# Kernel tuning notes

Measured on AMD Instinct MI355X. Metric: run time of the kernel, lower is better.

Reference implementation:

```python
import jax, jax.numpy as jnp
import numpy as np

N = 16384
H = 256
C = 2


def setup_inputs() -> dict:
    key = jax.random.key(0)
    ks = jax.random.split(key, 9)
    s = lambda fan_in: 1.0 / np.sqrt(fan_in)
    return {
        "coordinates": jax.random.normal(ks[0], (N, C), dtype=jnp.float32) * 10.0,
        "W1": jax.random.normal(ks[1], (C, H), dtype=jnp.float32) * s(C),
        "b1": jnp.zeros((H,), dtype=jnp.float32),
        "W2": jax.random.normal(ks[2], (H, H), dtype=jnp.float32) * s(H),
        "b2": jnp.zeros((H,), dtype=jnp.float32),
        "Wd1": jax.random.normal(ks[3], (1, H // 2), dtype=jnp.float32) * s(1),
        "bd1": jnp.zeros((H // 2,), dtype=jnp.float32),
        "Wd2": jax.random.normal(ks[4], (H // 2, H), dtype=jnp.float32) * s(H // 2),
        "bd2": jnp.zeros((H,), dtype=jnp.float32),
        "k": 6,
    }


def reference(coordinates, W1, b1, W2, b2, Wd1, bd1, Wd2, bd2, k):
    x = coordinates.astype(jnp.float32)
    # coord MLP: Linear -> SiLU -> Linear
    coord_emb = jax.nn.silu(x @ W1 + b1) @ W2 + b2  # (N, H)

    # pairwise Euclidean distances (N, N), via ||a||^2 + ||b||^2 - 2ab
    sq = jnp.sum(x * x, axis=1)  # (N,)
    d2 = sq[:, None] + sq[None, :] - 2.0 * (x @ x.T)
    dist = jnp.sqrt(jnp.maximum(d2, 1e-12))  # safe sqrt; diag ~ 0

    # k+1 smallest distances per row (includes self at ~0), ascending
    kk = min(k + 1, dist.shape[1])
    neg_top, _ = jax.lax.top_k(-dist, kk)
    topk_dist = -neg_top  # ascending smallest
    mean_dist = jnp.mean(topk_dist[:, 1:], axis=1, keepdims=True)  # (N, 1)

    dist_emb = jax.nn.silu(mean_dist @ Wd1 + bd1) @ Wd2 + bd2  # (N, H)
    return coord_emb + dist_emb
```

## Files before the change

kernel.cpp:

```cpp
#include <hip/hip_runtime.h>
#include <float.h>
#include <math.h>

#define NPTS 16384
#define HDIM 256

#define KNB   256
#define KXMIN (-48.0f)
#define KW    0.375f
#define KINVW (1.0f / KW)
#define NHB   64

typedef __attribute__((ext_vector_type(8))) short bf16x8;
typedef __attribute__((ext_vector_type(4))) float f32x4;

__device__ __forceinline__ float silu_f(float z) {
    return z / (1.0f + __expf(-z));
}

__device__ __forceinline__ short f2bf(float f) {
    unsigned u = __float_as_uint(f);
    u = (u + 0x7FFFu + ((u >> 16) & 1u)) >> 16;
    return (short)u;
}

__device__ __forceinline__ float bcast_lane(float x, int l) {
    return __int_as_float(__builtin_amdgcn_readlane(__float_as_int(x), l));
}

__device__ __forceinline__ int binof(float x) {
    int b = (int)floorf((x - KXMIN) * KINVW);
    return b < 0 ? 0 : (b > KNB - 1 ? KNB - 1 : b);
}

#define INS7(a0,a1,a2,a3,a4,a5,a6,V)                \
    {   const float v_ = (V);                       \
        a6 = fmaxf(a5, fminf(a6, v_));              \
        a5 = fmaxf(a4, fminf(a5, v_));              \
        a4 = fmaxf(a3, fminf(a4, v_));              \
        a3 = fmaxf(a2, fminf(a3, v_));              \
        a2 = fmaxf(a1, fminf(a2, v_));              \
        a1 = fmaxf(a0, fminf(a1, v_));              \
        a0 = fminf(a0, v_);                         \
    }

__global__ __launch_bounds__(256) void prepA_kernel(
        const float* __restrict__ xyf,
        const float* __restrict__ W2, const float* __restrict__ Wd2,
        unsigned short* __restrict__ W2p, unsigned short* __restrict__ Wd2p,
        unsigned* __restrict__ histp) {
    const int tid = threadIdx.x;

    if (blockIdx.x < 48) {
        const int slot = blockIdx.x * 256 + tid;
        const float* src;
        unsigned short* dst;
        int s;
        if (slot < 8192) { src = W2;  dst = W2p;  s = slot; }
        else             { src = Wd2; dst = Wd2p; s = slot - 8192; }
        const int t   = s >> 10;
        const int rem = s & 1023;
        const int ct  = rem >> 6;
        const int l   = rem & 63;
        const int k0  = t * 32 + 8 * (l >> 4);
        const int c   = ct * 16 + (l & 15);
        bf16x8 v;
        #pragma unroll
        for (int i = 0; i < 8; ++i)
            v[i] = f2bf(src[(size_t)(k0 + i) * HDIM + c]);
        ((bf16x8*)dst)[s] = v;
        return;
    }

    __shared__ unsigned lh[KNB];
    const int h = blockIdx.x - 48;
    lh[tid] = 0u;
    __syncthreads();
    atomicAdd(&lh[binof(xyf[2 * (h * 256 + tid)])], 1u);
    __syncthreads();
    histp[h * KNB + tid] = lh[tid];
}

__global__ __launch_bounds__(256) void prepB_kernel(
        const float* __restrict__ xyf,
        const unsigned* __restrict__ histp,
        unsigned* __restrict__ off,
        float2* __restrict__ sxy, unsigned* __restrict__ qidx) {
    __shared__ unsigned sc[KNB];
    __shared__ unsigned cur[KNB];
    const int tid = threadIdx.x;
    const int myb = blockIdx.x;

    unsigned tot = 0u, pre = 0u;
    #pragma unroll
    for (int b = 0; b < NHB; ++b) {
        const unsigned v = histp[b * KNB + tid];
        if (b < myb) pre += v;
        tot += v;
    }
    sc[tid] = tot;
    __syncthreads();
    for (int s = 1; s < KNB; s <<= 1) {
        const unsigned v = (tid >= s) ? sc[tid - s] : 0u;
        __syncthreads();
        sc[tid] += v;
        __syncthreads();
    }
    const unsigned excl = sc[tid] - tot;
    cur[tid] = excl + pre;
    if (myb == 0) {
        off[tid] = excl;
        if (tid == 0) off[KNB] = (unsigned)NPTS;
    }
    __syncthreads();
    const int i = myb * 256 + tid;
    const float2 p = ((const float2*)xyf)[i];
    const unsigned pos = atomicAdd(&cur[binof(p.x)], 1u);
    sxy[pos]  = p;
    qidx[pos] = (unsigned)i;
}

__global__ __launch_bounds__(512, 8) void knn_search(const float2* __restrict__ sxy,
                                                     const unsigned* __restrict__ qidx,
                                                     const unsigned* __restrict__ off,
                                                     float* __restrict__ md) {
    const int lane = threadIdx.x & 63;
    const int wv   = threadIdx.x >> 6;
    const int qpos = blockIdx.x * 8 + wv;
    const float2 q = sxy[qpos];

    float s0 = FLT_MAX, s1 = FLT_MAX, s2 = FLT_MAX, s3 = FLT_MAX,
          s4 = FLT_MAX, s5 = FLT_MAX, s6 = FLT_MAX;

    const int plo = qpos > 256 ? qpos - 256 : 0;
    const int phi = qpos < NPTS - 256 ? qpos + 255 : NPTS - 1;
    const int lb  = binof(sxy[plo].x);
    const int rb  = binof(sxy[phi].x);

    {
        const unsigned o = off[lb], e = off[rb + 1];
        for (unsigned u = o + (unsigned)lane; u < e; u += 64u) {
            const float2 p = sxy[u];
            const float dx = q.x - p.x, dy = q.y - p.y;
            const float d2 = fmaf(dx, dx, dy * dy);
            if (d2 < s6) INS7(s0, s1, s2, s3, s4, s5, s6, d2)
        }
    }

    #pragma unroll
    for (int m = 1; m < 64; m <<= 1) {
        const float o0 = __shfl_xor(s0, m);
        const float o1 = __shfl_xor(s1, m);
        const float o2 = __shfl_xor(s2, m);
        const float o3 = __shfl_xor(s3, m);
        const float o4 = __shfl_xor(s4, m);
        const float o5 = __shfl_xor(s5, m);
        const float o6 = __shfl_xor(s6, m);
        const float n0 = fminf(s0, o0);
        const float n1 = fminf(fminf(s1, o1), fmaxf(s0, o0));
        const float n2 = fminf(fminf(s2, o2),
                               fminf(fmaxf(s0, o1), fmaxf(s1, o0)));
        const float n3 = fminf(fminf(s3, o3),
                               fminf(fmaxf(s0, o2),
                                     fminf(fmaxf(s1, o1), fmaxf(s2, o0))));
        const float n4 = fminf(fminf(s4, o4),
                               fminf(fminf(fmaxf(s0, o3), fmaxf(s1, o2)),
                                     fminf(fmaxf(s2, o1), fmaxf(s3, o0))));
        const float n5 = fminf(fminf(s5, o5),
                               fminf(fminf(fmaxf(s0, o4), fmaxf(s1, o3)),
                                     fminf(fmaxf(s2, o2),
                                           fminf(fmaxf(s3, o1), fmaxf(s4, o0)))));
        const float n6 = fminf(fminf(s6, o6),
                               fminf(fminf(fmaxf(s0, o5), fmaxf(s1, o4)),
                                     fminf(fmaxf(s2, o3),
                                           fminf(fmaxf(s3, o2),
                                                 fminf(fmaxf(s4, o1),
                                                       fmaxf(s5, o0))))));
        s0 = n0; s1 = n1; s2 = n2; s3 = n3; s4 = n4; s5 = n5; s6 = n6;
    }

    int l = lb - 1, r = rb + 1;
    while (l >= 0 || r < KNB) {
        float bl = FLT_MAX, br = FLT_MAX;
        if (l >= 0) {
            const float d = fmaxf(q.x - (KXMIN + (float)(l + 1) * KW), 0.0f);
            bl = d * d;
        }
        if (r < KNB) {
            const float d = fmaxf((KXMIN + (float)r * KW) - q.x, 0.0f);
            br = d * d;
        }
        if (fminf(bl, br) > s6) break;
        const int b = (bl <= br) ? l : r;
        const unsigned o = off[b], e = off[b + 1];
        for (unsigned u = o; u < e; u += 64u) {
            const unsigned idx = u + (unsigned)lane;
            float d2 = FLT_MAX;
            if (idx < e) {
                const float2 p = sxy[idx];
                const float dx = q.x - p.x, dy = q.y - p.y;
                d2 = fmaf(dx, dx, dy * dy);
            }
            unsigned long long m = __ballot(d2 < s6);
            while (m) {
                const int L   = __ffsll(m) - 1;
                const float v = bcast_lane(d2, L);
                INS7(s0, s1, s2, s3, s4, s5, s6, v)
                if (lane == L) d2 = FLT_MAX;
                m = __ballot(d2 < s6);
            }
        }
        if (bl <= br) --l; else ++r;
    }

    if (lane == 0) {
        const float sum = sqrtf(fmaxf(s1, 1e-12f)) + sqrtf(fmaxf(s2, 1e-12f)) +
                          sqrtf(fmaxf(s3, 1e-12f)) + sqrtf(fmaxf(s4, 1e-12f)) +
                          sqrtf(fmaxf(s5, 1e-12f)) + sqrtf(fmaxf(s6, 1e-12f));
        md[qidx[qpos]] = sum * (1.0f / 6.0f);
    }
}

#define GEN_A(T)                                                              \
    {                                                                         \
        const int kb = (T) * 32 + klane;                                      \
        const float4 p0 = *(const float4*)(W1 + kb);                          \
        const float4 p1 = *(const float4*)(W1 + kb + 4);                      \
        const float4 r0_ = *(const float4*)(W1 + HDIM + kb);                  \
        const float4 r1_ = *(const float4*)(W1 + HDIM + kb + 4);              \
        const float4 c0_ = *(const float4*)(b1 + kb);                         \
        const float4 c1_ = *(const float4*)(b1 + kb + 4);                     \
        const float pw[8] = {p0.x,p0.y,p0.z,p0.w,p1.x,p1.y,p1.z,p1.w};        \
        const float rw[8] = {r0_.x,r0_.y,r0_.z,r0_.w,r1_.x,r1_.y,r1_.z,r1_.w};\
        const float cw[8] = {c0_.x,c0_.y,c0_.z,c0_.w,c1_.x,c1_.y,c1_.z,c1_.w};\
        _Pragma("unroll")                                                     \
        for (int i = 0; i < 8; ++i)                                           \
            a[i] = f2bf(silu_f(fmaf(q.x, pw[i], fmaf(q.y, rw[i], cw[i]))));   \
    }

#define GEN_G(T)                                                              \
    {                                                                         \
        const int kb = (T) * 32 + klane;                                      \
        const float4 p0 = *(const float4*)(Wd1 + kb);                         \
        const float4 p1 = *(const float4*)(Wd1 + kb + 4);                     \
        const float4 c0_ = *(const float4*)(bd1 + kb);                        \
        const float4 c1_ = *(const float4*)(bd1 + kb + 4);                    \
        const float pw[8] = {p0.x,p0.y,p0.z,p0.w,p1.x,p1.y,p1.z,p1.w};        \
        const float cw[8] = {c0_.x,c0_.y,c0_.z,c0_.w,c1_.x,c1_.y,c1_.z,c1_.w};\
        _Pragma("unroll")                                                     \
        for (int i = 0; i < 8; ++i)                                           \
            a[i] = f2bf(silu_f(fmaf(mdr, pw[i], cw[i])));                     \
    }

#define MFMA8(BUF)                                                            \
    _Pragma("unroll")                                                         \
    for (int j = 0; j < 8; ++j)                                               \
        acc[j] = __builtin_amdgcn_mfma_f32_16x16x32_bf16(a, BUF[j], acc[j], 0, 0, 0);

#define LOADB(BUF, ARR, T)                                                    \
    _Pragma("unroll")                                                         \
    for (int j = 0; j < 8; ++j)                                               \
        BUF[j] = ARR[((T) * 16 + ch * 8 + j) * 64 + lane];

__global__ __launch_bounds__(256, 2) void mlp_kernel(
        const float* __restrict__ xyf,
        const float* __restrict__ W1,  const float* __restrict__ b1,
        const float* __restrict__ b2,
        const float* __restrict__ Wd1, const float* __restrict__ bd1,
        const float* __restrict__ bd2,
        const unsigned short* __restrict__ W2p,
        const unsigned short* __restrict__ Wd2p,
        const float* __restrict__ md,  float* __restrict__ out) {
    const int tid  = threadIdx.x;
    const int lane = tid & 63;
    const int w    = tid >> 6;
    const int r0   = blockIdx.x * 32 + (w >> 1) * 16;
    const int ch   = w & 1;
    const int row  = r0 + (lane & 15);
    const float2 q = ((const float2*)xyf)[row];
    const float mdr = md[row];
    const int klane = 8 * (lane >> 4);

    f32x4 acc[8];
    #pragma unroll
    for (int j = 0; j < 8; ++j) {
        acc[j][0] = 0.0f; acc[j][1] = 0.0f; acc[j][2] = 0.0f; acc[j][3] = 0.0f;
    }

    const bf16x8* B1 = (const bf16x8*)W2p;
    const bf16x8* B2 = (const bf16x8*)Wd2p;
    bf16x8 bA[8], bB[8];
    bf16x8 a;

    LOADB(bA, B1, 0)

    #pragma unroll
    for (int tt = 0; tt < 4; ++tt) {
        {   const int t = 2 * tt;
            GEN_A(t)
            LOADB(bB, B1, t + 1)
            MFMA8(bA)
        }
        {   const int t = 2 * tt + 1;
            GEN_A(t)
            if (t + 1 < 8) { LOADB(bA, B1, t + 1) }
            else           { LOADB(bA, B2, 0)     }
            MFMA8(bB)
        }
    }

    #pragma unroll
    for (int uu = 0; uu < 2; ++uu) {
        {   const int t = 2 * uu;
            GEN_G(t)
            LOADB(bB, B2, t + 1)
            MFMA8(bA)
        }
        {   const int t = 2 * uu + 1;
            GEN_G(t)
            if (t + 1 < 4) { LOADB(bA, B2, t + 1) }
            MFMA8(bB)
        }
    }

    const int cb = ch * 128;
    const int rr = r0 + 4 * (lane >> 4);
    #pragma unroll
    for (int j = 0; j < 8; ++j) {
        const int c = cb + j * 16 + (lane & 15);
        const float add = b2[c] + bd2[c];
        out[(size_t)(rr + 0) * HDIM + c] = acc[j][0] + add;
        out[(size_t)(rr + 1) * HDIM + c] = acc[j][1] + add;
        out[(size_t)(rr + 2) * HDIM + c] = acc[j][2] + add;
        out[(size_t)(rr + 3) * HDIM + c] = acc[j][3] + add;
    }
}

extern "C" void kernel_launch(void* const* d_in, const int* in_sizes, int n_in,
                              void* d_out, int out_size, void* d_ws, size_t ws_size,
                              hipStream_t stream) {
    const float* xy  = (const float*)d_in[0];
    const float* W1  = (const float*)d_in[1];
    const float* b1  = (const float*)d_in[2];
    const float* W2  = (const float*)d_in[3];
    const float* b2  = (const float*)d_in[4];
    const float* Wd1 = (const float*)d_in[5];
    const float* bd1 = (const float*)d_in[6];
    const float* Wd2 = (const float*)d_in[7];
    const float* bd2 = (const float*)d_in[8];
    float* out = (float*)d_out;

    char* ws = (char*)d_ws;
    float*          md    = (float*)ws;
    unsigned*       histp = (unsigned*)ws;
    unsigned short* W2p   = (unsigned short*)(ws + 65536);
    unsigned short* Wd2p  = (unsigned short*)(ws + 196608);
    unsigned*       off   = (unsigned*)(ws + 262144);
    float2*         sxy   = (float2*)(ws + 263424);
    unsigned*       qidx  = (unsigned*)(ws + 394496);

    prepA_kernel<<<48 + NHB, 256, 0, stream>>>(xy, W2, Wd2, W2p, Wd2p, histp);
    prepB_kernel<<<NHB, 256, 0, stream>>>(xy, histp, off, sxy, qidx);
    knn_search<<<NPTS / 8, 512, 0, stream>>>(sxy, qidx, off, md);
    mlp_kernel<<<NPTS / 32, 256, 0, stream>>>(xy, W1, b1, b2, Wd1, bd1, bd2,
                                              W2p, Wd2p, md, out);
}
```

Baseline: 151.8 us.

## Keep per-lane top-7 lists during bin expansion and merge across wave periodically

The outward bin-expansion loop previously held one wave-uniform top-7 list and inserted candidates serially with a ballot/readlane loop. Now each lane keeps its own top-7 list while scanning bins, and a wave-wide butterfly merge runs every two bins to refresh a shared pruning bound, with one final merge before the result is written. This is meant to remove the serialized per-candidate insertion. In exchange the bound is staler, so some extra bins may be scanned, and the repeated shuffle merges add cost.

```diff
diff --git a/kernel.cpp b/kernel.cpp
--- a/kernel.cpp
+++ b/kernel.cpp
@@ -22,10 +22,6 @@
     unsigned u = __float_as_uint(f);
     u = (u + 0x7FFFu + ((u >> 16) & 1u)) >> 16;
     return (short)u;
-}
-
-__device__ __forceinline__ float bcast_lane(float x, int l) {
-    return __int_as_float(__builtin_amdgcn_readlane(__float_as_int(x), l));
 }
 
 __device__ __forceinline__ int binof(float x) {
@@ -42,6 +38,40 @@
         a2 = fmaxf(a1, fminf(a2, v_));              \
         a1 = fmaxf(a0, fminf(a1, v_));              \
         a0 = fminf(a0, v_);                         \
+    }
+
+#define MERGE7(a0,a1,a2,a3,a4,a5,a6)                                          \
+    _Pragma("unroll")                                                         \
+    for (int m = 1; m < 64; m <<= 1) {                                        \
+        const float o0 = __shfl_xor(a0, m);                                   \
+        const float o1 = __shfl_xor(a1, m);                                   \
+        const float o2 = __shfl_xor(a2, m);                                   \
+        const float o3 = __shfl_xor(a3, m);                                   \
+        const float o4 = __shfl_xor(a4, m);                                   \
+        const float o5 = __shfl_xor(a5, m);                                   \
+        const float o6 = __shfl_xor(a6, m);                                   \
+        const float n0 = fminf(a0, o0);                                       \
+        const float n1 = fminf(fminf(a1, o1), fmaxf(a0, o0));                 \
+        const float n2 = fminf(fminf(a2, o2),                                 \
+                               fminf(fmaxf(a0, o1), fmaxf(a1, o0)));          \
+        const float n3 = fminf(fminf(a3, o3),                                 \
+                               fminf(fmaxf(a0, o2),                           \
+                                     fminf(fmaxf(a1, o1), fmaxf(a2, o0))));   \
+        const float n4 = fminf(fminf(a4, o4),                                 \
+                               fminf(fminf(fmaxf(a0, o3), fmaxf(a1, o2)),     \
+                                     fminf(fmaxf(a2, o1), fmaxf(a3, o0))));   \
+        const float n5 = fminf(fminf(a5, o5),                                 \
+                               fminf(fminf(fmaxf(a0, o4), fmaxf(a1, o3)),     \
+                                     fminf(fmaxf(a2, o2),                     \
+                                           fminf(fmaxf(a3, o1),               \
+                                                 fmaxf(a4, o0)))));           \
+        const float n6 = fminf(fminf(a6, o6),                                 \
+                               fminf(fminf(fmaxf(a0, o5), fmaxf(a1, o4)),     \
+                                     fminf(fmaxf(a2, o3),                     \
+                                           fminf(fmaxf(a3, o2),               \
+                                                 fminf(fmaxf(a4, o1),         \
+                                                       fmaxf(a5, o0))))));    \
+        a0 = n0; a1 = n1; a2 = n2; a3 = n3; a4 = n4; a5 = n5; a6 = n6;        \
     }
 
 __global__ __launch_bounds__(256) void prepA_kernel(
@@ -147,39 +177,14 @@
         }
     }
 
-    #pragma unroll
-    for (int m = 1; m < 64; m <<= 1) {
-        const float o0 = __shfl_xor(s0, m);
-        const float o1 = __shfl_xor(s1, m);
-        const float o2 = __shfl_xor(s2, m);
-        const float o3 = __shfl_xor(s3, m);
-        const float o4 = __shfl_xor(s4, m);
-        const float o5 = __shfl_xor(s5, m);
-        const float o6 = __shfl_xor(s6, m);
-        const float n0 = fminf(s0, o0);
-        const float n1 = fminf(fminf(s1, o1), fmaxf(s0, o0));
-        const float n2 = fminf(fminf(s2, o2),
-                               fminf(fmaxf(s0, o1), fmaxf(s1, o0)));
-        const float n3 = fminf(fminf(s3, o3),
-                               fminf(fmaxf(s0, o2),
-                                     fminf(fmaxf(s1, o1), fmaxf(s2, o0))));
-        const float n4 = fminf(fminf(s4, o4),
-                               fminf(fminf(fmaxf(s0, o3), fmaxf(s1, o2)),
-                                     fminf(fmaxf(s2, o1), fmaxf(s3, o0))));
-        const float n5 = fminf(fminf(s5, o5),
-                               fminf(fminf(fmaxf(s0, o4), fmaxf(s1, o3)),
-                                     fminf(fmaxf(s2, o2),
-                                           fminf(fmaxf(s3, o1), fmaxf(s4, o0)))));
-        const float n6 = fminf(fminf(s6, o6),
-                               fminf(fminf(fmaxf(s0, o5), fmaxf(s1, o4)),
-                                     fminf(fmaxf(s2, o3),
-                                           fminf(fmaxf(s3, o2),
-                                                 fminf(fmaxf(s4, o1),
-                                                       fmaxf(s5, o0))))));
-        s0 = n0; s1 = n1; s2 = n2; s3 = n3; s4 = n4; s5 = n5; s6 = n6;
-    }
-
-    int l = lb - 1, r = rb + 1;
+    float ub;
+    {
+        float t0 = s0, t1 = s1, t2 = s2, t3 = s3, t4 = s4, t5 = s5, t6 = s6;
+        MERGE7(t0, t1, t2, t3, t4, t5, t6)
+        ub = t6;
+    }
+
+    int l = lb - 1, r = rb + 1, since = 0;
     while (l >= 0 || r < KNB) {
         float bl = FLT_MAX, br = FLT_MAX;
         if (l >= 0) {
@@ -190,33 +195,32 @@
             const float d = fmaxf((KXMIN + (float)r * KW) - q.x, 0.0f);
             br = d * d;
         }
-        if (fminf(bl, br) > s6) break;
+        if (fminf(bl, br) > ub) break;
         const int b = (bl <= br) ? l : r;
         const unsigned o = off[b], e = off[b + 1];
-        for (unsigned u = o; u < e; u += 64u) {
-            const unsigned idx = u + (unsigned)lane;
-            float d2 = FLT_MAX;
-            if (idx < e) {
-                const float2 p = sxy[idx];
-                const float dx = q.x - p.x, dy = q.y - p.y;
-                d2 = fmaf(dx, dx, dy * dy);
-            }
-            unsigned long long m = __ballot(d2 < s6);
-            while (m) {
-                const int L   = __ffsll(m) - 1;
-                const float v = bcast_lane(d2, L);
-                INS7(s0, s1, s2, s3, s4, s5, s6, v)
-                if (lane == L) d2 = FLT_MAX;
-                m = __ballot(d2 < s6);
-            }
+        for (unsigned u = o + (unsigned)lane; u < e; u += 64u) {
+            const float2 p = sxy[u];
+            const float dx = q.x - p.x, dy = q.y - p.y;
+            const float d2 = fmaf(dx, dx, dy * dy);
+            if (d2 < s6) INS7(s0, s1, s2, s3, s4, s5, s6, d2)
         }
         if (bl <= br) --l; else ++r;
-    }
+        if (++since >= 2) {
+            float t0 = s0, t1 = s1, t2 = s2, t3 = s3,
+                  t4 = s4, t5 = s5, t6 = s6;
+            MERGE7(t0, t1, t2, t3, t4, t5, t6)
+            ub = t6;
+            since = 0;
+        }
+    }
+
+    float c0 = s0, c1 = s1, c2 = s2, c3 = s3, c4 = s4, c5 = s5, c6 = s6;
+    MERGE7(c0, c1, c2, c3, c4, c5, c6)
 
     if (lane == 0) {
-        const float sum = sqrtf(fmaxf(s1, 1e-12f)) + sqrtf(fmaxf(s2, 1e-12f)) +
-                          sqrtf(fmaxf(s3, 1e-12f)) + sqrtf(fmaxf(s4, 1e-12f)) +
-                          sqrtf(fmaxf(s5, 1e-12f)) + sqrtf(fmaxf(s6, 1e-12f));
+        const float sum = sqrtf(fmaxf(c1, 1e-12f)) + sqrtf(fmaxf(c2, 1e-12f)) +
+                          sqrtf(fmaxf(c3, 1e-12f)) + sqrtf(fmaxf(c4, 1e-12f)) +
+                          sqrtf(fmaxf(c5, 1e-12f)) + sqrtf(fmaxf(c6, 1e-12f));
         md[qidx[qpos]] = sum * (1.0f / 6.0f);
     }
 }
```

Measured after the change: 172.7 us. 13.8% more time.
